# Kernel optimization log

Hardware: AMD Instinct MI355X
Metric: run time of the kernel (lower is better)

## Reference

```python
import jax, jax.numpy as jnp
import numpy as np

B, H, W, C, G = 4, 56, 56, 256, 16
K = 9  # 3x3 deformable kernel
GC = C // G


def _ln(x, g, b, eps=1e-5):
    mu = jnp.mean(x, axis=-1, keepdims=True)
    var = jnp.mean(jnp.square(x - mu), axis=-1, keepdims=True)
    return (x - mu) * jax.lax.rsqrt(var + eps) * g + b


def _gelu(x):
    return jax.nn.gelu(x, approximate=False)  # torch nn.GELU default = exact erf


def _dcnv3_core(x, offset, mask):
    # x: [B,H,W,C]; offset: [B,H,W,G*K*2] (x,y per point); mask: [B,H,W,G,K] softmaxed over K
    xg = x.reshape(B, H * W, G, GC)
    off = offset.reshape(B, H, W, G, K, 2)
    dy, dx = jnp.meshgrid(jnp.arange(-1.0, 2.0), jnp.arange(-1.0, 2.0), indexing="ij")
    dx = dx.reshape(K).astype(x.dtype)
    dy = dy.reshape(K).astype(x.dtype)
    gx = jnp.arange(W, dtype=x.dtype)[None, None, :, None, None]
    gy = jnp.arange(H, dtype=x.dtype)[None, :, None, None, None]
    # sampling locations in unpadded pixel coords (zeros outside image == F.pad + zero grid_sample)
    px = gx + dx + off[..., 0]  # [B,H,W,G,K]
    py = gy + dy + off[..., 1]

    def flat(p):  # [B,H,W,G,K] -> [B, H*W*K, G]
        return p.transpose(0, 1, 2, 4, 3).reshape(B, H * W * K, G)

    pxf, pyf = flat(px), flat(py)
    x0 = jnp.floor(pxf)
    y0 = jnp.floor(pyf)
    acc = jnp.zeros((B, H * W * K, G, GC), x.dtype)
    for cx, cy in ((x0, y0), (x0 + 1, y0), (x0, y0 + 1), (x0 + 1, y0 + 1)):
        wgt = (1 - jnp.abs(pxf - cx)) * (1 - jnp.abs(pyf - cy))
        valid = ((cx >= 0) & (cx < W) & (cy >= 0) & (cy < H)).astype(x.dtype)
        idx = (jnp.clip(cy, 0, H - 1).astype(jnp.int32) * W
               + jnp.clip(cx, 0, W - 1).astype(jnp.int32))[..., None]  # [B,HWK,G,1]
        v = jnp.take_along_axis(xg, idx, axis=1)  # [B,HWK,G,GC]
        acc = acc + (wgt * valid)[..., None] * v
    mf = flat(mask)[..., None]  # [B,HWK,G,1]
    out = (acc * mf).reshape(B, H * W, K, G, GC).sum(axis=2)
    return out.reshape(B, H, W, C)


def _dcn(x, w_in, b_in, w_dw, b_dw, ln_dw_g, ln_dw_b, w_off, b_off,
         w_mask, b_mask, w_out, b_out):
    xp = x @ w_in + b_in  # input projection (value branch)
    x1 = jax.lax.conv_general_dilated(
        x, w_dw, window_strides=(1, 1), padding="SAME",
        dimension_numbers=("NHWC", "HWIO", "NHWC"), feature_group_count=C) + b_dw
    x1 = _gelu(_ln(x1, ln_dw_g, ln_dw_b))  # dw_conv -> LN -> GELU
    offset = x1 @ w_off + b_off  # [B,H,W,G*K*2]
    mask = jax.nn.softmax((x1 @ w_mask + b_mask).reshape(B, H, W, G, K), axis=-1)
    y = _dcnv3_core(xp, offset, mask)
    return y @ w_out + b_out


def _block(x, w_in, b_in, w_dw, b_dw, ln_dw_g, ln_dw_b, w_off, b_off,
           w_mask, b_mask, w_out, b_out, ln1_g, ln1_b,
           w_fc1, b_fc1, w_fc2, b_fc2, ln2_g, ln2_b, gamma1, gamma2):
    # post_norm=True: x = x + gamma1*LN1(dcn(x)); x = x + gamma2*LN2(mlp(x))
    y = _dcn(x, w_in, b_in, w_dw, b_dw, ln_dw_g, ln_dw_b, w_off, b_off,
             w_mask, b_mask, w_out, b_out)
    x = x + gamma1 * _ln(y, ln1_g, ln1_b)
    m = _gelu(x @ w_fc1 + b_fc1) @ w_fc2 + b_fc2  # MLP (dropout = identity)
    x = x + gamma2 * _ln(m, ln2_g, ln2_b)
    return x


def setup_inputs() -> dict:
    key = jax.random.key(0)
    ks = jax.random.split(key, 9)
    f = jnp.float32

    def rn(k, shape, s=0.02):
        return jax.random.normal(k, shape, dtype=f) * s

    return {
        "x": jax.random.normal(ks[0], (B, H, W, C), dtype=f),
        "w_in": rn(ks[1], (C, C)), "b_in": jnp.zeros((C,), f),
        "w_dw": rn(ks[2], (3, 3, 1, C), 0.1), "b_dw": jnp.zeros((C,), f),
        "ln_dw_g": jnp.ones((C,), f), "ln_dw_b": jnp.zeros((C,), f),
        "w_off": rn(ks[3], (C, G * K * 2)), "b_off": jnp.zeros((G * K * 2,), f),
        "w_mask": rn(ks[4], (C, G * K)), "b_mask": jnp.zeros((G * K,), f),
        "w_out": rn(ks[5], (C, C)), "b_out": jnp.zeros((C,), f),
        "ln1_g": jnp.ones((C,), f), "ln1_b": jnp.zeros((C,), f),
        "w_fc1": rn(ks[6], (C, C)), "b_fc1": jnp.zeros((C,), f),
        "w_fc2": rn(ks[7], (C, C)), "b_fc2": jnp.zeros((C,), f),
        "ln2_g": jnp.ones((C,), f), "ln2_b": jnp.zeros((C,), f),
        "gamma1": jnp.ones((C,), f), "gamma2": jnp.ones((C,), f),
    }


def reference(x, w_in, b_in, w_dw, b_dw, ln_dw_g, ln_dw_b, w_off, b_off,
              w_mask, b_mask, w_out, b_out, ln1_g, ln1_b,
              w_fc1, b_fc1, w_fc2, b_fc2, ln2_g, ln2_b, gamma1, gamma2):
    return _block(x, w_in, b_in, w_dw, b_dw, ln_dw_g, ln_dw_b, w_off, b_off,
                  w_mask, b_mask, w_out, b_out, ln1_g, ln1_b,
                  w_fc1, b_fc1, w_fc2, b_fc2, ln2_g, ln2_b, gamma1, gamma2)
```

## Files before the change

### kernel.cpp

```cpp
#include <hip/hip_runtime.h>
#include <math.h>

typedef unsigned short u16;
typedef unsigned int u32;
typedef __attribute__((ext_vector_type(8))) short short8;
typedef __attribute__((ext_vector_type(4))) float f32x4;

#define NB 4
#define NH 56
#define NW 56
#define HW2 (NH*NW)
#define NPIX (NB*HW2)

__device__ __forceinline__ u16 f2b(float f) {
  union { float f; u32 u; } a; a.f = f;
  return (u16)((a.u + 0x7FFFu + ((a.u >> 16) & 1u)) >> 16);
}
__device__ __forceinline__ float b2f(u16 v) {
  union { u32 u; float f; } a; a.u = ((u32)v) << 16; return a.f;
}
__device__ __forceinline__ float gelu_exact(float v) {
  return 0.5f * v * (1.0f + erff(v * 0.70710678118654752f));
}
__device__ __forceinline__ int xcd_swz(int bid, int nwg) {
  const int q = nwg >> 3, r = nwg & 7, x = bid & 7, j = bid >> 3;
  return (x < r ? x * (q + 1) : r * (q + 1) + (x - r) * q) + j;
}
__device__ __forceinline__ u32 swz(int r, int b) {
  return (u32)(r * 512 + ((b ^ (r & 7)) << 4));
}

__global__ __launch_bounds__(256) void k1_kernel(
    const float* __restrict__ w_in, const float* __restrict__ w_out,
    const float* __restrict__ w_fc1, const float* __restrict__ w_fc2,
    const float* __restrict__ w_off, const float* __restrict__ w_mask,
    const float* __restrict__ b_off, const float* __restrict__ b_mask,
    u16* __restrict__ wT, float* __restrict__ bias_cat,
    const float* __restrict__ xf, const float* __restrict__ wdw,
    const float* __restrict__ bdw, const float* __restrict__ lng,
    const float* __restrict__ lnb, u16* __restrict__ x1)
{
  const int blk = blockIdx.x, t = threadIdx.x;
  if (blk < 1456) {
    const float* src; int n, N;
    if      (blk < 256)  { src = w_in;   n = blk;        N = 256; }
    else if (blk < 512)  { src = w_out;  n = blk - 256;  N = 256; }
    else if (blk < 768)  { src = w_fc1;  n = blk - 512;  N = 256; }
    else if (blk < 1024) { src = w_fc2;  n = blk - 768;  N = 256; }
    else if (blk < 1312) { src = w_off;  n = blk - 1024; N = 288; }
    else                 { src = w_mask; n = blk - 1312; N = 144; }
    wT[blk * 256 + t] = f2b(src[t * N + n]);
  } else if (blk == 1456) {
    for (int j = t; j < 432; j += 256)
      bias_cat[j] = (j < 288) ? b_off[j] : b_mask[j - 288];
  } else {
    const int pb = xcd_swz(blk - 1457, 3136);
    const int p = pb * 4 + (t >> 6);
    const int lane = t & 63, c0 = lane * 4;
    const int bb = p / HW2, hw = p - bb * HW2;
    const int h = hw / NW, w = hw - h * NW;
    float4 bd = *(const float4*)(bdw + c0);
    float a0 = bd.x, a1 = bd.y, a2 = bd.z, a3 = bd.w;
    #pragma unroll
    for (int kh = 0; kh < 3; ++kh) {
      const int hh = h + kh - 1;
      if ((unsigned)hh >= NH) continue;
      #pragma unroll
      for (int kw = 0; kw < 3; ++kw) {
        const int ww = w + kw - 1;
        if ((unsigned)ww >= NW) continue;
        float4 v = *(const float4*)(xf + (size_t)(bb * HW2 + hh * NW + ww) * 256 + c0);
        float4 wv = *(const float4*)(wdw + (kh * 3 + kw) * 256 + c0);
        a0 += v.x * wv.x; a1 += v.y * wv.y;
        a2 += v.z * wv.z; a3 += v.w * wv.w;
      }
    }
    float s1 = a0 + a1 + a2 + a3;
    float s2 = a0 * a0 + a1 * a1 + a2 * a2 + a3 * a3;
    #pragma unroll
    for (int d = 1; d < 64; d <<= 1) { s1 += __shfl_xor(s1, d); s2 += __shfl_xor(s2, d); }
    const float mu = s1 * (1.0f / 256.0f);
    const float var = s2 * (1.0f / 256.0f) - mu * mu;
    const float rs = rsqrtf(var + 1e-5f);
    float4 lg4 = *(const float4*)(lng + c0);
    float4 lb4 = *(const float4*)(lnb + c0);
    ushort4 o;
    o.x = f2b(gelu_exact((a0 - mu) * rs * lg4.x + lb4.x));
    o.y = f2b(gelu_exact((a1 - mu) * rs * lg4.y + lb4.y));
    o.z = f2b(gelu_exact((a2 - mu) * rs * lg4.z + lb4.z));
    o.w = f2b(gelu_exact((a3 - mu) * rs * lg4.w + lb4.w));
    *(ushort4*)(x1 + (size_t)p * 256 + c0) = o;
  }
}

template<int AF32>
__device__ __forceinline__ void gemm64_body(
    const void* __restrict__ Asrc, const u16* __restrict__ Brows,
    const float* __restrict__ bias, u16* __restrict__ Cout,
    int Ntot, int m0, int n0, char* As, char* Bs, int t)
{
  if (AF32) {
    const int r = t >> 2;
    const float4* src = (const float4*)((const float*)Asrc + (size_t)(m0 + r) * 256);
    #pragma unroll
    for (int i = 0; i < 16; ++i) {
      const int f4 = (t & 3) + i * 4;
      float4 v = src[f4];
      uint2 pk;
      pk.x = (u32)f2b(v.x) | ((u32)f2b(v.y) << 16);
      pk.y = (u32)f2b(v.z) | ((u32)f2b(v.w) << 16);
      *(uint2*)(As + swz(r, f4 >> 1) + (f4 & 1) * 8) = pk;
    }
  } else {
    const int r = t >> 2, c0 = t & 3;
    const u16* Ag = (const u16*)Asrc + (size_t)(m0 + r) * 256;
    #pragma unroll
    for (int i = 0; i < 8; ++i) {
      const int b = c0 + i * 4;
      *(uint4*)(As + swz(r, b)) = *(const uint4*)(Ag + b * 8);
    }
  }
  {
    const int r = t >> 2, c0 = t & 3;
    const int nrow = n0 + r;
    const u16* Bg = Brows + (size_t)nrow * 256;
    const bool bok = nrow < Ntot;
    #pragma unroll
    for (int i = 0; i < 8; ++i) {
      const int b = c0 + i * 4;
      uint4 bv = make_uint4(0u, 0u, 0u, 0u);
      if (bok) bv = *(const uint4*)(Bg + b * 8);
      *(uint4*)(Bs + swz(r, b)) = bv;
    }
  }
  __syncthreads();
  const int l = t & 63, w = t >> 6;
  const int wm = (w >> 1) << 5, wn = (w & 1) << 5;
  const int lr = l & 15, lk = l >> 4;
  const int ra0 = wm + lr, ra1 = wm + 16 + lr;
  const int rb0 = wn + lr, rb1 = wn + 16 + lr;
  f32x4 acc00 = {}, acc01 = {}, acc10 = {}, acc11 = {};
  #pragma unroll
  for (int ks = 0; ks < 8; ++ks) {
    const int bb = ks * 4 + lk;
    short8 a0 = *(const short8*)(As + swz(ra0, bb));
    short8 a1 = *(const short8*)(As + swz(ra1, bb));
    short8 b0 = *(const short8*)(Bs + swz(rb0, bb));
    short8 b1 = *(const short8*)(Bs + swz(rb1, bb));
    acc00 = __builtin_amdgcn_mfma_f32_16x16x32_bf16(a0, b0, acc00, 0, 0, 0);
    acc01 = __builtin_amdgcn_mfma_f32_16x16x32_bf16(a0, b1, acc01, 0, 0, 0);
    acc10 = __builtin_amdgcn_mfma_f32_16x16x32_bf16(a1, b0, acc10, 0, 0, 0);
    acc11 = __builtin_amdgcn_mfma_f32_16x16x32_bf16(a1, b1, acc11, 0, 0, 0);
  }
  const f32x4 accs[2][2] = {{acc00, acc01}, {acc10, acc11}};
  #pragma unroll
  for (int mi = 0; mi < 2; ++mi)
    #pragma unroll
    for (int ni = 0; ni < 2; ++ni) {
      const int col = n0 + wn + ni * 16 + lr;
      if (col < Ntot) {
        const float bv = bias[col];
        #pragma unroll
        for (int r4 = 0; r4 < 4; ++r4) {
          const int row = m0 + wm + mi * 16 + lk * 4 + r4;
          Cout[(size_t)row * Ntot + col] = f2b(accs[mi][ni][r4] + bv);
        }
      }
    }
}

__global__ __launch_bounds__(256) void k2_kernel(
    const float* __restrict__ xf, const u16* __restrict__ x1,
    const u16* __restrict__ wT, const float* __restrict__ b_in,
    const float* __restrict__ bcat, u16* __restrict__ xp_bf,
    u16* __restrict__ omb)
{
  __shared__ u16 lds[32768];
  char* As = (char*)lds;
  char* Bs = (char*)(lds + 16384);
  const int t = threadIdx.x;
  if (blockIdx.x < 784) {
    const int sb = xcd_swz(blockIdx.x, 784);
    const int m0 = (sb >> 2) * 64, n0 = (sb & 3) * 64;
    gemm64_body<1>(xf, wT, b_in, xp_bf, 256, m0, n0, As, Bs, t);
  } else {
    const int sb = xcd_swz((int)blockIdx.x - 784, 1372);
    const int m0 = (sb / 7) * 64, n0 = (sb % 7) * 64;
    gemm64_body<0>(x1, wT + 1024 * 256, bcat, omb, 432, m0, n0, As, Bs, t);
  }
}

__global__ __launch_bounds__(512) void dcn_tail_kernel(
    const u16* __restrict__ xp, const u16* __restrict__ omb,
    const u16* __restrict__ wT, const float* __restrict__ x,
    const float* __restrict__ b_out, const float* __restrict__ gamma1,
    const float* __restrict__ ln1g, const float* __restrict__ ln1b,
    const float* __restrict__ b_fc1, const float* __restrict__ b_fc2,
    const float* __restrict__ gamma2, const float* __restrict__ ln2g,
    const float* __restrict__ ln2b, float* __restrict__ out)
{
  __shared__ u16 As[32 * 256];
  __shared__ u16 lom[32 * 432];
  __shared__ float redS[32][8], redQ[32][8];
  const int t = threadIdx.x;
  const int blk = xcd_swz(blockIdx.x, 392);
  const int p0 = blk * 32;

  for (int i = t; i < 1728; i += 512) {
    const int row = i / 54, u = i - row * 54;
    *(uint4*)(lom + row * 432 + u * 8) =
        *(const uint4*)(omb + (size_t)(p0 + row) * 432 + u * 8);
  }
  __syncthreads();

  {
    const int lp = t >> 4, g = t & 15;
    const int p = p0 + lp;
    const int bb = p / HW2, hw = p - bb * HW2;
    const int h = hw / NW, w = hw - h * NW;
    const u16* off = lom + lp * 432 + g * 18;
    const u16* mk  = lom + lp * 432 + 288 + g * 9;
    float lg[9];
    float mx = -1e30f;
    #pragma unroll
    for (int k = 0; k < 9; ++k) { lg[k] = b2f(mk[k]); mx = fmaxf(mx, lg[k]); }
    float se = 0.0f;
    #pragma unroll
    for (int k = 0; k < 9; ++k) { lg[k] = __expf(lg[k] - mx); se += lg[k]; }
    const float inv = 1.0f / se;
    float a[16];
    #pragma unroll
    for (int j = 0; j < 16; ++j) a[j] = 0.f;
    const u16* gbase = xp + (size_t)bb * HW2 * 256 + g * 16;
    auto corner = [&](int cx, int cy, float wt) {
      if (cx < 0 || cx >= NW || cy < 0 || cy >= NH) return;
      const u16* vp = gbase + (size_t)(cy * NW + cx) * 256;
      uint4 v0 = *(const uint4*)vp;
      uint4 v1 = *(const uint4*)(vp + 8);
      const u32 wv[8] = {v0.x, v0.y, v0.z, v0.w, v1.x, v1.y, v1.z, v1.w};
      #pragma unroll
      for (int j = 0; j < 8; ++j) {
        union { u32 u; float f; } lo, hi;
        lo.u = wv[j] << 16; hi.u = wv[j] & 0xffff0000u;
        a[2 * j]     += wt * lo.f;
        a[2 * j + 1] += wt * hi.f;
      }
    };
    #pragma unroll
    for (int k = 0; k < 9; ++k) {
      const float px = (float)(w + (k % 3) - 1) + b2f(off[2 * k]);
      const float py = (float)(h + (k / 3) - 1) + b2f(off[2 * k + 1]);
      const float fx = floorf(px), fy = floorf(py);
      const int ix = (int)fx, iy = (int)fy;
      const float ax = px - fx, ay = py - fy;
      const float mwt = lg[k] * inv;
      corner(ix,     iy,     (1.0f - ax) * (1.0f - ay) * mwt);
      corner(ix + 1, iy,     ax * (1.0f - ay) * mwt);
      corner(ix,     iy + 1, (1.0f - ax) * ay * mwt);
      corner(ix + 1, iy + 1, ax * ay * mwt);
    }
    u16 tmp[16];
    #pragma unroll
    for (int j = 0; j < 16; ++j) tmp[j] = f2b(a[j]);
    const int u0 = g * 2;
    *(uint4*)((char*)As + lp * 512 + (((u0    ) ^ (lp & 7)) << 4)) = *(const uint4*)(tmp);
    *(uint4*)((char*)As + lp * 512 + (((u0 + 1) ^ (lp & 7)) << 4)) = *(const uint4*)(tmp + 8);
  }
  __syncthreads();

  const int l = t & 63, w8 = t >> 6;
  const int lr = l & 15, lk = l >> 4;
  const int colb = w8 * 32 + lr;
  f32x4 acc[2][2];
  auto do_gemm = [&](const u16* Bt) {
    #pragma unroll
    for (int mi = 0; mi < 2; ++mi)
      #pragma unroll
      for (int ni = 0; ni < 2; ++ni) acc[mi][ni] = (f32x4){0.f, 0.f, 0.f, 0.f};
    const u16* Bbase = Bt + (size_t)(w8 * 32 + lr) * 256 + lk * 8;
    #pragma unroll
    for (int ks = 0; ks < 8; ++ks) {
      short8 a0 = *(const short8*)((char*)As + swz(lr,      ks * 4 + lk));
      short8 a1 = *(const short8*)((char*)As + swz(16 + lr, ks * 4 + lk));
      #pragma unroll
      for (int ni = 0; ni < 2; ++ni) {
        short8 b = *(const short8*)(Bbase + ni * 16 * 256 + ks * 32);
        acc[0][ni] = __builtin_amdgcn_mfma_f32_16x16x32_bf16(a0, b, acc[0][ni], 0, 0, 0);
        acc[1][ni] = __builtin_amdgcn_mfma_f32_16x16x32_bf16(a1, b, acc[1][ni], 0, 0, 0);
      }
    }
  };
  auto lds_write_b16 = [&](int row, int col, u16 v) {
    *(u16*)((char*)As + row * 512 + (((col >> 3) ^ (row & 7)) << 4) + (col & 7) * 2) = v;
  };
  auto ln_reduce = [&](const float bv[2]) {
    float s1[2][4], s2[2][4];
    #pragma unroll
    for (int mi = 0; mi < 2; ++mi)
      #pragma unroll
      for (int r4 = 0; r4 < 4; ++r4) {
        float s = 0.f, q = 0.f;
        #pragma unroll
        for (int ni = 0; ni < 2; ++ni) {
          const float v = acc[mi][ni][r4] + bv[ni];
          s += v; q += v * v;
        }
        s1[mi][r4] = s; s2[mi][r4] = q;
      }
    #pragma unroll
    for (int d = 1; d < 16; d <<= 1)
      #pragma unroll
      for (int mi = 0; mi < 2; ++mi)
        #pragma unroll
        for (int r4 = 0; r4 < 4; ++r4) {
          s1[mi][r4] += __shfl_xor(s1[mi][r4], d);
          s2[mi][r4] += __shfl_xor(s2[mi][r4], d);
        }
    if (lr == 0) {
      #pragma unroll
      for (int mi = 0; mi < 2; ++mi)
        #pragma unroll
        for (int r4 = 0; r4 < 4; ++r4) {
          const int rl = mi * 16 + lk * 4 + r4;
          redS[rl][w8] = s1[mi][r4];
          redQ[rl][w8] = s2[mi][r4];
        }
    }
    __syncthreads();
  };
  auto row_stats = [&](int rl, float& mu, float& rs) {
    float S = 0.f, Q = 0.f;
    #pragma unroll
    for (int j = 0; j < 8; ++j) { S += redS[rl][j]; Q += redQ[rl][j]; }
    mu = S * (1.0f / 256.0f);
    const float var = Q * (1.0f / 256.0f) - mu * mu;
    rs = rsqrtf(var + 1e-5f);
  };

  do_gemm(wT + 256 * 256);
  float bv1[2] = {b_out[colb], b_out[colb + 16]};
  ln_reduce(bv1);

  float x2r[2][4][2];
  {
    const float gm[2]  = {gamma1[colb], gamma1[colb + 16]};
    const float lgv[2] = {ln1g[colb],   ln1g[colb + 16]};
    const float lbv[2] = {ln1b[colb],   ln1b[colb + 16]};
    #pragma unroll
    for (int mi = 0; mi < 2; ++mi)
      #pragma unroll
      for (int r4 = 0; r4 < 4; ++r4) {
        const int rl = mi * 16 + lk * 4 + r4;
        float mu, rs; row_stats(rl, mu, rs);
        const int row = p0 + rl;
        #pragma unroll
        for (int ni = 0; ni < 2; ++ni) {
          const float v = acc[mi][ni][r4] + bv1[ni];
          const float o = x[(size_t)row * 256 + colb + ni * 16]
                        + gm[ni] * ((v - mu) * rs * lgv[ni] + lbv[ni]);
          x2r[mi][r4][ni] = o;
          lds_write_b16(rl, colb + ni * 16, f2b(o));
        }
      }
  }
  __syncthreads();

  do_gemm(wT + 512 * 256);
  float m1v[2][4][2];
  const float bf1[2] = {b_fc1[colb], b_fc1[colb + 16]};
  #pragma unroll
  for (int mi = 0; mi < 2; ++mi)
    #pragma unroll
    for (int r4 = 0; r4 < 4; ++r4)
      #pragma unroll
      for (int ni = 0; ni < 2; ++ni)
        m1v[mi][r4][ni] = gelu_exact(acc[mi][ni][r4] + bf1[ni]);
  __syncthreads();
  #pragma unroll
  for (int mi = 0; mi < 2; ++mi)
    #pragma unroll
    for (int r4 = 0; r4 < 4; ++r4) {
      const int rl = mi * 16 + lk * 4 + r4;
      #pragma unroll
      for (int ni = 0; ni < 2; ++ni)
        lds_write_b16(rl, colb + ni * 16, f2b(m1v[mi][r4][ni]));
    }
  __syncthreads();

  do_gemm(wT + 768 * 256);
  float bv3[2] = {b_fc2[colb], b_fc2[colb + 16]};
  ln_reduce(bv3);
  {
    const float gm[2]  = {gamma2[colb], gamma2[colb + 16]};
    const float lgv[2] = {ln2g[colb],   ln2g[colb + 16]};
    const float lbv[2] = {ln2b[colb],   ln2b[colb + 16]};
    #pragma unroll
    for (int mi = 0; mi < 2; ++mi)
      #pragma unroll
      for (int r4 = 0; r4 < 4; ++r4) {
        const int rl = mi * 16 + lk * 4 + r4;
        float mu, rs; row_stats(rl, mu, rs);
        const int row = p0 + rl;
        #pragma unroll
        for (int ni = 0; ni < 2; ++ni) {
          const float v = acc[mi][ni][r4] + bv3[ni];
          out[(size_t)row * 256 + colb + ni * 16] =
              x2r[mi][r4][ni] + gm[ni] * ((v - mu) * rs * lgv[ni] + lbv[ni]);
        }
      }
  }
}

static constexpr size_t OFF_WT  = 0;
static constexpr size_t OFF_BC  = 745472;
static constexpr size_t OFF_XP  = 747520;
static constexpr size_t OFF_X1  = 7170048;
static constexpr size_t OFF_OMB = 13592576;

extern "C" void kernel_launch(void* const* d_in, const int* in_sizes, int n_in,
                              void* d_out, int out_size, void* d_ws, size_t ws_size,
                              hipStream_t stream)
{
  const float* x      = (const float*)d_in[0];
  const float* w_in   = (const float*)d_in[1];
  const float* b_in   = (const float*)d_in[2];
  const float* w_dw   = (const float*)d_in[3];
  const float* b_dw   = (const float*)d_in[4];
  const float* ln_dw_g= (const float*)d_in[5];
  const float* ln_dw_b= (const float*)d_in[6];
  const float* w_off  = (const float*)d_in[7];
  const float* b_off  = (const float*)d_in[8];
  const float* w_mask = (const float*)d_in[9];
  const float* b_mask = (const float*)d_in[10];
  const float* w_out  = (const float*)d_in[11];
  const float* b_out  = (const float*)d_in[12];
  const float* ln1_g  = (const float*)d_in[13];
  const float* ln1_b  = (const float*)d_in[14];
  const float* w_fc1  = (const float*)d_in[15];
  const float* b_fc1  = (const float*)d_in[16];
  const float* w_fc2  = (const float*)d_in[17];
  const float* b_fc2  = (const float*)d_in[18];
  const float* ln2_g  = (const float*)d_in[19];
  const float* ln2_b  = (const float*)d_in[20];
  const float* gamma1 = (const float*)d_in[21];
  const float* gamma2 = (const float*)d_in[22];
  float* out = (float*)d_out;

  char* ws = (char*)d_ws;
  u16*   wT    = (u16*)  (ws + OFF_WT);
  float* bcat  = (float*)(ws + OFF_BC);
  u16*   xp_bf = (u16*)  (ws + OFF_XP);
  u16*   x1    = (u16*)  (ws + OFF_X1);
  u16*   omb   = (u16*)  (ws + OFF_OMB);

  k1_kernel<<<dim3(1457 + 3136), 256, 0, stream>>>(
      w_in, w_out, w_fc1, w_fc2, w_off, w_mask, b_off, b_mask, wT, bcat,
      x, w_dw, b_dw, ln_dw_g, ln_dw_b, x1);
  k2_kernel<<<dim3(784 + 1372), 256, 0, stream>>>(
      x, x1, wT, b_in, bcat, xp_bf, omb);
  dcn_tail_kernel<<<dim3(392), 512, 0, stream>>>(
      xp_bf, omb, wT, x, b_out, gamma1, ln1_g, ln1_b, b_fc1, b_fc2,
      gamma2, ln2_g, ln2_b, out);
}
```

Before: 88.09 us.

## Halve tail-kernel tile to 16 pixels per block with 256 threads

The fused DCN tail kernel now handles 16 pixels per block with 4 waves instead of 32 pixels with 8 waves, launching 784 blocks instead of 392. Each wave now computes a 16x64 output slice with four MFMA accumulators in place of a 32x32 slice. The aim is to fill all compute units on the 256-CU device, since 392 blocks left many idle. In exchange, each block re-reads the weight matrices from global or L2 for fewer rows, roughly doubling weight traffic per pixel.

```diff
diff --git a/kernel.cpp b/kernel.cpp
--- a/kernel.cpp
+++ b/kernel.cpp
@@ -190,7 +190,7 @@
   }
 }
 
-__global__ __launch_bounds__(512) void dcn_tail_kernel(
+__global__ __launch_bounds__(256) void dcn_tail_kernel(
     const u16* __restrict__ xp, const u16* __restrict__ omb,
     const u16* __restrict__ wT, const float* __restrict__ x,
     const float* __restrict__ b_out, const float* __restrict__ gamma1,
@@ -199,14 +199,14 @@
     const float* __restrict__ gamma2, const float* __restrict__ ln2g,
     const float* __restrict__ ln2b, float* __restrict__ out)
 {
-  __shared__ u16 As[32 * 256];
-  __shared__ u16 lom[32 * 432];
-  __shared__ float redS[32][8], redQ[32][8];
+  __shared__ u16 As[16 * 256];
+  __shared__ u16 lom[16 * 432];
+  __shared__ float redS[16][4], redQ[16][4];
   const int t = threadIdx.x;
-  const int blk = xcd_swz(blockIdx.x, 392);
-  const int p0 = blk * 32;
-
-  for (int i = t; i < 1728; i += 512) {
+  const int blk = xcd_swz(blockIdx.x, 784);
+  const int p0 = blk * 16;
+
+  for (int i = t; i < 864; i += 256) {
     const int row = i / 54, u = i - row * 54;
     *(uint4*)(lom + row * 432 + u * 8) =
         *(const uint4*)(omb + (size_t)(p0 + row) * 432 + u * 8);
@@ -268,146 +268,143 @@
   }
   __syncthreads();
 
-  const int l = t & 63, w8 = t >> 6;
+  const int l = t & 63, w4 = t >> 6;
   const int lr = l & 15, lk = l >> 4;
-  const int colb = w8 * 32 + lr;
-  f32x4 acc[2][2];
+  const int colb = w4 * 64 + lr;
+  f32x4 acc[4];
   auto do_gemm = [&](const u16* Bt) {
     #pragma unroll
-    for (int mi = 0; mi < 2; ++mi)
-      #pragma unroll
-      for (int ni = 0; ni < 2; ++ni) acc[mi][ni] = (f32x4){0.f, 0.f, 0.f, 0.f};
-    const u16* Bbase = Bt + (size_t)(w8 * 32 + lr) * 256 + lk * 8;
+    for (int ni = 0; ni < 4; ++ni) acc[ni] = (f32x4){0.f, 0.f, 0.f, 0.f};
+    const u16* Bbase = Bt + (size_t)(w4 * 64 + lr) * 256 + lk * 8;
     #pragma unroll
     for (int ks = 0; ks < 8; ++ks) {
-      short8 a0 = *(const short8*)((char*)As + swz(lr,      ks * 4 + lk));
-      short8 a1 = *(const short8*)((char*)As + swz(16 + lr, ks * 4 + lk));
-      #pragma unroll
-      for (int ni = 0; ni < 2; ++ni) {
+      short8 a0 = *(const short8*)((char*)As + swz(lr, ks * 4 + lk));
+      #pragma unroll
+      for (int ni = 0; ni < 4; ++ni) {
         short8 b = *(const short8*)(Bbase + ni * 16 * 256 + ks * 32);
-        acc[0][ni] = __builtin_amdgcn_mfma_f32_16x16x32_bf16(a0, b, acc[0][ni], 0, 0, 0);
-        acc[1][ni] = __builtin_amdgcn_mfma_f32_16x16x32_bf16(a1, b, acc[1][ni], 0, 0, 0);
+        acc[ni] = __builtin_amdgcn_mfma_f32_16x16x32_bf16(a0, b, acc[ni], 0, 0, 0);
       }
     }
   };
   auto lds_write_b16 = [&](int row, int col, u16 v) {
     *(u16*)((char*)As + row * 512 + (((col >> 3) ^ (row & 7)) << 4) + (col & 7) * 2) = v;
   };
-  auto ln_reduce = [&](const float bv[2]) {
-    float s1[2][4], s2[2][4];
-    #pragma unroll
-    for (int mi = 0; mi < 2; ++mi)
+  auto ln_reduce = [&](const float bv[4]) {
+    float s1[4], s2[4];
+    #pragma unroll
+    for (int r4 = 0; r4 < 4; ++r4) {
+      float s = 0.f, q = 0.f;
+      #pragma unroll
+      for (int ni = 0; ni < 4; ++ni) {
+        const float v = acc[ni][r4] + bv[ni];
+        s += v; q += v * v;
+      }
+      s1[r4] = s; s2[r4] = q;
+    }
+    #pragma unroll
+    for (int d = 1; d < 16; d <<= 1)
       #pragma unroll
       for (int r4 = 0; r4 < 4; ++r4) {
-        float s = 0.f, q = 0.f;
-        #pragma unroll
-        for (int ni = 0; ni < 2; ++ni) {
-          const float v = acc[mi][ni][r4] + bv[ni];
-          s += v; q += v * v;
-        }
-        s1[mi][r4] = s; s2[mi][r4] = q;
-      }
-    #pragma unroll
-    for (int d = 1; d < 16; d <<= 1)
-      #pragma unroll
-      for (int mi = 0; mi < 2; ++mi)
-        #pragma unroll
-        for (int r4 = 0; r4 < 4; ++r4) {
-          s1[mi][r4] += __shfl_xor(s1[mi][r4], d);
-          s2[mi][r4] += __shfl_xor(s2[mi][r4], d);
-        }
+        s1[r4] += __shfl_xor(s1[r4], d);
+        s2[r4] += __shfl_xor(s2[r4], d);
+      }
     if (lr == 0) {
       #pragma unroll
-      for (int mi = 0; mi < 2; ++mi)
-        #pragma unroll
-        for (int r4 = 0; r4 < 4; ++r4) {
-          const int rl = mi * 16 + lk * 4 + r4;
-          redS[rl][w8] = s1[mi][r4];
-          redQ[rl][w8] = s2[mi][r4];
-        }
+      for (int r4 = 0; r4 < 4; ++r4) {
+        const int rl = lk * 4 + r4;
+        redS[rl][w4] = s1[r4];
+        redQ[rl][w4] = s2[r4];
+      }
     }
     __syncthreads();
   };
   auto row_stats = [&](int rl, float& mu, float& rs) {
-    float S = 0.f, Q = 0.f;
-    #pragma unroll
-    for (int j = 0; j < 8; ++j) { S += redS[rl][j]; Q += redQ[rl][j]; }
+    const float S = redS[rl][0] + redS[rl][1] + redS[rl][2] + redS[rl][3];
+    const float Q = redQ[rl][0] + redQ[rl][1] + redQ[rl][2] + redQ[rl][3];
     mu = S * (1.0f / 256.0f);
     const float var = Q * (1.0f / 256.0f) - mu * mu;
     rs = rsqrtf(var + 1e-5f);
   };
 
   do_gemm(wT + 256 * 256);
-  float bv1[2] = {b_out[colb], b_out[colb + 16]};
+  float bv1[4];
+  #pragma unroll
+  for (int ni = 0; ni < 4; ++ni) bv1[ni] = b_out[colb + ni * 16];
   ln_reduce(bv1);
 
-  float x2r[2][4][2];
+  float x2r[4][4];
   {
-    const float gm[2]  = {gamma1[colb], gamma1[colb + 16]};
-    const float lgv[2] = {ln1g[colb],   ln1g[colb + 16]};
-    const float lbv[2] = {ln1b[colb],   ln1b[colb + 16]};
-    #pragma unroll
-    for (int mi = 0; mi < 2; ++mi)
-      #pragma unroll
-      for (int r4 = 0; r4 < 4; ++r4) {
-        const int rl = mi * 16 + lk * 4 + r4;
-        float mu, rs; row_stats(rl, mu, rs);
-        const int row = p0 + rl;
-        #pragma unroll
-        for (int ni = 0; ni < 2; ++ni) {
-          const float v = acc[mi][ni][r4] + bv1[ni];
-          const float o = x[(size_t)row * 256 + colb + ni * 16]
-                        + gm[ni] * ((v - mu) * rs * lgv[ni] + lbv[ni]);
-          x2r[mi][r4][ni] = o;
-          lds_write_b16(rl, colb + ni * 16, f2b(o));
-        }
-      }
+    float gm[4], lgv[4], lbv[4];
+    #pragma unroll
+    for (int ni = 0; ni < 4; ++ni) {
+      gm[ni]  = gamma1[colb + ni * 16];
+      lgv[ni] = ln1g[colb + ni * 16];
+      lbv[ni] = ln1b[colb + ni * 16];
+    }
+    #pragma unroll
+    for (int r4 = 0; r4 < 4; ++r4) {
+      const int rl = lk * 4 + r4;
+      float mu, rs; row_stats(rl, mu, rs);
+      const int row = p0 + rl;
+      #pragma unroll
+      for (int ni = 0; ni < 4; ++ni) {
+        const float v = acc[ni][r4] + bv1[ni];
+        const float o = x[(size_t)row * 256 + colb + ni * 16]
+                      + gm[ni] * ((v - mu) * rs * lgv[ni] + lbv[ni]);
+        x2r[r4][ni] = o;
+        lds_write_b16(rl, colb + ni * 16, f2b(o));
+      }
+    }
   }
   __syncthreads();
 
   do_gemm(wT + 512 * 256);
-  float m1v[2][4][2];
-  const float bf1[2] = {b_fc1[colb], b_fc1[colb + 16]};
+  float m1v[4][4];
+  {
+    float bf1[4];
+    #pragma unroll
+    for (int ni = 0; ni < 4; ++ni) bf1[ni] = b_fc1[colb + ni * 16];
+    #pragma unroll
+    for (int r4 = 0; r4 < 4; ++r4)
+      #pragma unroll
+      for (int ni = 0; ni < 4; ++ni)
+        m1v[r4][ni] = gelu_exact(acc[ni][r4] + bf1[ni]);
+  }
+  __syncthreads();
   #pragma unroll
-  for (int mi = 0; mi < 2; ++mi)
-    #pragma unroll
-    for (int r4 = 0; r4 < 4; ++r4)
-      #pragma unroll
-      for (int ni = 0; ni < 2; ++ni)
-        m1v[mi][r4][ni] = gelu_exact(acc[mi][ni][r4] + bf1[ni]);
-  __syncthreads();
+  for (int r4 = 0; r4 < 4; ++r4) {
+    const int rl = lk * 4 + r4;
+    #pragma unroll
+    for (int ni = 0; ni < 4; ++ni)
+      lds_write_b16(rl, colb + ni * 16, f2b(m1v[r4][ni]));
+  }
+  __syncthreads();
+
+  do_gemm(wT + 768 * 256);
+  float bv3[4];
   #pragma unroll
-  for (int mi = 0; mi < 2; ++mi)
-    #pragma unroll
-    for (int r4 = 0; r4 < 4; ++r4) {
-      const int rl = mi * 16 + lk * 4 + r4;
-      #pragma unroll
-      for (int ni = 0; ni < 2; ++ni)
-        lds_write_b16(rl, colb + ni * 16, f2b(m1v[mi][r4][ni]));
-    }
-  __syncthreads();
-
-  do_gemm(wT + 768 * 256);
-  float bv3[2] = {b_fc2[colb], b_fc2[colb + 16]};
+  for (int ni = 0; ni < 4; ++ni) bv3[ni] = b_fc2[colb + ni * 16];
   ln_reduce(bv3);
   {
-    const float gm[2]  = {gamma2[colb], gamma2[colb + 16]};
-    const float lgv[2] = {ln2g[colb],   ln2g[colb + 16]};
-    const float lbv[2] = {ln2b[colb],   ln2b[colb + 16]};
-    #pragma unroll
-    for (int mi = 0; mi < 2; ++mi)
-      #pragma unroll
-      for (int r4 = 0; r4 < 4; ++r4) {
-        const int rl = mi * 16 + lk * 4 + r4;
-        float mu, rs; row_stats(rl, mu, rs);
-        const int row = p0 + rl;
-        #pragma unroll
-        for (int ni = 0; ni < 2; ++ni) {
-          const float v = acc[mi][ni][r4] + bv3[ni];
-          out[(size_t)row * 256 + colb + ni * 16] =
-              x2r[mi][r4][ni] + gm[ni] * ((v - mu) * rs * lgv[ni] + lbv[ni]);
-        }
-      }
+    float gm[4], lgv[4], lbv[4];
+    #pragma unroll
+    for (int ni = 0; ni < 4; ++ni) {
+      gm[ni]  = gamma2[colb + ni * 16];
+      lgv[ni] = ln2g[colb + ni * 16];
+      lbv[ni] = ln2b[colb + ni * 16];
+    }
+    #pragma unroll
+    for (int r4 = 0; r4 < 4; ++r4) {
+      const int rl = lk * 4 + r4;
+      float mu, rs; row_stats(rl, mu, rs);
+      const int row = p0 + rl;
+      #pragma unroll
+      for (int ni = 0; ni < 4; ++ni) {
+        const float v = acc[ni][r4] + bv3[ni];
+        out[(size_t)row * 256 + colb + ni * 16] =
+            x2r[r4][ni] + gm[ni] * ((v - mu) * rs * lgv[ni] + lbv[ni]);
+      }
+    }
   }
 }
 
@@ -458,7 +455,7 @@
       x, w_dw, b_dw, ln_dw_g, ln_dw_b, x1);
   k2_kernel<<<dim3(784 + 1372), 256, 0, stream>>>(
       x, x1, wT, b_in, bcat, xp_bf, omb);
-  dcn_tail_kernel<<<dim3(392), 512, 0, stream>>>(
+  dcn_tail_kernel<<<dim3(784), 256, 0, stream>>>(
       xp_bf, omb, wT, x, b_out, gamma1, ln1_g, ln1_b, b_fc1, b_fc2,
       gamma2, ln2_g, ln2_b, out);
 }
```

Result: slower. 109.3 us (+24.0%).

## Double tail kernel threads to 1024, splitting gather and GEMM columns finer

Applied to the files above, without the earlier changes.

The DCN tail kernel now runs 1024 threads per block instead of 512. Each bilinear-gather thread handles half of a group's 16 channels (one 16-byte load per corner), and each wave in the fused GEMM/LN chain owns 16 output columns instead of 32. The reduction scratch grows to 16 partials per row. This raises memory-level parallelism for the gather with only 392 blocks, at the cost of more LN reduction work, more redundant offset/softmax math per thread, and larger blocks that may limit occupancy.

```diff
diff --git a/kernel.cpp b/kernel.cpp
--- a/kernel.cpp
+++ b/kernel.cpp
@@ -190,7 +190,7 @@
   }
 }
 
-__global__ __launch_bounds__(512) void dcn_tail_kernel(
+__global__ __launch_bounds__(1024) void dcn_tail_kernel(
     const u16* __restrict__ xp, const u16* __restrict__ omb,
     const u16* __restrict__ wT, const float* __restrict__ x,
     const float* __restrict__ b_out, const float* __restrict__ gamma1,
@@ -201,12 +201,12 @@
 {
   __shared__ u16 As[32 * 256];
   __shared__ u16 lom[32 * 432];
-  __shared__ float redS[32][8], redQ[32][8];
+  __shared__ float redS[32][16], redQ[32][16];
   const int t = threadIdx.x;
   const int blk = xcd_swz(blockIdx.x, 392);
   const int p0 = blk * 32;
 
-  for (int i = t; i < 1728; i += 512) {
+  for (int i = t; i < 1728; i += 1024) {
     const int row = i / 54, u = i - row * 54;
     *(uint4*)(lom + row * 432 + u * 8) =
         *(const uint4*)(omb + (size_t)(p0 + row) * 432 + u * 8);
@@ -214,7 +214,8 @@
   __syncthreads();
 
   {
-    const int lp = t >> 4, g = t & 15;
+    const int lp = t >> 5, gh = t & 31;
+    const int g = gh >> 1, hf = gh & 1;
     const int p = p0 + lp;
     const int bb = p / HW2, hw = p - bb * HW2;
     const int h = hw / NW, w = hw - h * NW;
@@ -228,18 +229,14 @@
     #pragma unroll
     for (int k = 0; k < 9; ++k) { lg[k] = __expf(lg[k] - mx); se += lg[k]; }
     const float inv = 1.0f / se;
-    float a[16];
-    #pragma unroll
-    for (int j = 0; j < 16; ++j) a[j] = 0.f;
-    const u16* gbase = xp + (size_t)bb * HW2 * 256 + g * 16;
+    float a[8] = {0.f,0.f,0.f,0.f,0.f,0.f,0.f,0.f};
+    const u16* gbase = xp + (size_t)bb * HW2 * 256 + g * 16 + hf * 8;
     auto corner = [&](int cx, int cy, float wt) {
       if (cx < 0 || cx >= NW || cy < 0 || cy >= NH) return;
-      const u16* vp = gbase + (size_t)(cy * NW + cx) * 256;
-      uint4 v0 = *(const uint4*)vp;
-      uint4 v1 = *(const uint4*)(vp + 8);
-      const u32 wv[8] = {v0.x, v0.y, v0.z, v0.w, v1.x, v1.y, v1.z, v1.w};
-      #pragma unroll
-      for (int j = 0; j < 8; ++j) {
+      uint4 v = *(const uint4*)(gbase + (size_t)(cy * NW + cx) * 256);
+      const u32 wv[4] = {v.x, v.y, v.z, v.w};
+      #pragma unroll
+      for (int j = 0; j < 4; ++j) {
         union { u32 u; float f; } lo, hi;
         lo.u = wv[j] << 16; hi.u = wv[j] & 0xffff0000u;
         a[2 * j]     += wt * lo.f;
@@ -259,53 +256,41 @@
       corner(ix,     iy + 1, (1.0f - ax) * ay * mwt);
       corner(ix + 1, iy + 1, ax * ay * mwt);
     }
-    u16 tmp[16];
-    #pragma unroll
-    for (int j = 0; j < 16; ++j) tmp[j] = f2b(a[j]);
-    const int u0 = g * 2;
-    *(uint4*)((char*)As + lp * 512 + (((u0    ) ^ (lp & 7)) << 4)) = *(const uint4*)(tmp);
-    *(uint4*)((char*)As + lp * 512 + (((u0 + 1) ^ (lp & 7)) << 4)) = *(const uint4*)(tmp + 8);
-  }
-  __syncthreads();
-
-  const int l = t & 63, w8 = t >> 6;
+    u16 tmp[8];
+    #pragma unroll
+    for (int j = 0; j < 8; ++j) tmp[j] = f2b(a[j]);
+    *(uint4*)((char*)As + lp * 512 + ((gh ^ (lp & 7)) << 4)) = *(const uint4*)(tmp);
+  }
+  __syncthreads();
+
+  const int l = t & 63, wv16 = t >> 6;
   const int lr = l & 15, lk = l >> 4;
-  const int colb = w8 * 32 + lr;
-  f32x4 acc[2][2];
+  const int colb = wv16 * 16 + lr;
+  f32x4 acc[2];
   auto do_gemm = [&](const u16* Bt) {
-    #pragma unroll
-    for (int mi = 0; mi < 2; ++mi)
-      #pragma unroll
-      for (int ni = 0; ni < 2; ++ni) acc[mi][ni] = (f32x4){0.f, 0.f, 0.f, 0.f};
-    const u16* Bbase = Bt + (size_t)(w8 * 32 + lr) * 256 + lk * 8;
+    acc[0] = (f32x4){0.f, 0.f, 0.f, 0.f};
+    acc[1] = (f32x4){0.f, 0.f, 0.f, 0.f};
+    const u16* Bbase = Bt + (size_t)colb * 256 + lk * 8;
     #pragma unroll
     for (int ks = 0; ks < 8; ++ks) {
       short8 a0 = *(const short8*)((char*)As + swz(lr,      ks * 4 + lk));
       short8 a1 = *(const short8*)((char*)As + swz(16 + lr, ks * 4 + lk));
-      #pragma unroll
-      for (int ni = 0; ni < 2; ++ni) {
-        short8 b = *(const short8*)(Bbase + ni * 16 * 256 + ks * 32);
-        acc[0][ni] = __builtin_amdgcn_mfma_f32_16x16x32_bf16(a0, b, acc[0][ni], 0, 0, 0);
-        acc[1][ni] = __builtin_amdgcn_mfma_f32_16x16x32_bf16(a1, b, acc[1][ni], 0, 0, 0);
-      }
+      short8 b = *(const short8*)(Bbase + ks * 32);
+      acc[0] = __builtin_amdgcn_mfma_f32_16x16x32_bf16(a0, b, acc[0], 0, 0, 0);
+      acc[1] = __builtin_amdgcn_mfma_f32_16x16x32_bf16(a1, b, acc[1], 0, 0, 0);
     }
   };
   auto lds_write_b16 = [&](int row, int col, u16 v) {
     *(u16*)((char*)As + row * 512 + (((col >> 3) ^ (row & 7)) << 4) + (col & 7) * 2) = v;
   };
-  auto ln_reduce = [&](const float bv[2]) {
+  auto ln_reduce = [&](float bv) {
     float s1[2][4], s2[2][4];
     #pragma unroll
     for (int mi = 0; mi < 2; ++mi)
       #pragma unroll
       for (int r4 = 0; r4 < 4; ++r4) {
-        float s = 0.f, q = 0.f;
-        #pragma unroll
-        for (int ni = 0; ni < 2; ++ni) {
-          const float v = acc[mi][ni][r4] + bv[ni];
-          s += v; q += v * v;
-        }
-        s1[mi][r4] = s; s2[mi][r4] = q;
+        const float v = acc[mi][r4] + bv;
+        s1[mi][r4] = v; s2[mi][r4] = v * v;
       }
     #pragma unroll
     for (int d = 1; d < 16; d <<= 1)
@@ -322,8 +307,8 @@
         #pragma unroll
         for (int r4 = 0; r4 < 4; ++r4) {
           const int rl = mi * 16 + lk * 4 + r4;
-          redS[rl][w8] = s1[mi][r4];
-          redQ[rl][w8] = s2[mi][r4];
+          redS[rl][wv16] = s1[mi][r4];
+          redQ[rl][wv16] = s2[mi][r4];
         }
     }
     __syncthreads();
@@ -331,21 +316,21 @@
   auto row_stats = [&](int rl, float& mu, float& rs) {
     float S = 0.f, Q = 0.f;
     #pragma unroll
-    for (int j = 0; j < 8; ++j) { S += redS[rl][j]; Q += redQ[rl][j]; }
+    for (int j = 0; j < 16; ++j) { S += redS[rl][j]; Q += redQ[rl][j]; }
     mu = S * (1.0f / 256.0f);
     const float var = Q * (1.0f / 256.0f) - mu * mu;
     rs = rsqrtf(var + 1e-5f);
   };
 
   do_gemm(wT + 256 * 256);
-  float bv1[2] = {b_out[colb], b_out[colb + 16]};
+  const float bv1 = b_out[colb];
   ln_reduce(bv1);
 
-  float x2r[2][4][2];
+  float x2r[2][4];
   {
-    const float gm[2]  = {gamma1[colb], gamma1[colb + 16]};
-    const float lgv[2] = {ln1g[colb],   ln1g[colb + 16]};
-    const float lbv[2] = {ln1b[colb],   ln1b[colb + 16]};
+    const float gm  = gamma1[colb];
+    const float lgv = ln1g[colb];
+    const float lbv = ln1b[colb];
     #pragma unroll
     for (int mi = 0; mi < 2; ++mi)
       #pragma unroll
@@ -353,47 +338,42 @@
         const int rl = mi * 16 + lk * 4 + r4;
         float mu, rs; row_stats(rl, mu, rs);
         const int row = p0 + rl;
-        #pragma unroll
-        for (int ni = 0; ni < 2; ++ni) {
-          const float v = acc[mi][ni][r4] + bv1[ni];
-          const float o = x[(size_t)row * 256 + colb + ni * 16]
-                        + gm[ni] * ((v - mu) * rs * lgv[ni] + lbv[ni]);
-          x2r[mi][r4][ni] = o;
-          lds_write_b16(rl, colb + ni * 16, f2b(o));
-        }
+        const float v = acc[mi][r4] + bv1;
+        const float o = x[(size_t)row * 256 + colb]
+                      + gm * ((v - mu) * rs * lgv + lbv);
+        x2r[mi][r4] = o;
+        lds_write_b16(rl, colb, f2b(o));
       }
   }
   __syncthreads();
 
   do_gemm(wT + 512 * 256);
-  float m1v[2][4][2];
-  const float bf1[2] = {b_fc1[colb], b_fc1[colb + 16]};
+  float m1v[2][4];
+  {
+    const float bf1 = b_fc1[colb];
+    #pragma unroll
+    for (int mi = 0; mi < 2; ++mi)
+      #pragma unroll
+      for (int r4 = 0; r4 < 4; ++r4)
+        m1v[mi][r4] = gelu_exact(acc[mi][r4] + bf1);
+  }
+  __syncthreads();
   #pragma unroll
   for (int mi = 0; mi < 2; ++mi)
     #pragma unroll
-    for (int r4 = 0; r4 < 4; ++r4)
-      #pragma unroll
-      for (int ni = 0; ni < 2; ++ni)
-        m1v[mi][r4][ni] = gelu_exact(acc[mi][ni][r4] + bf1[ni]);
-  __syncthreads();
-  #pragma unroll
-  for (int mi = 0; mi < 2; ++mi)
-    #pragma unroll
     for (int r4 = 0; r4 < 4; ++r4) {
       const int rl = mi * 16 + lk * 4 + r4;
-      #pragma unroll
-      for (int ni = 0; ni < 2; ++ni)
-        lds_write_b16(rl, colb + ni * 16, f2b(m1v[mi][r4][ni]));
+      lds_write_b16(rl, colb, f2b(m1v[mi][r4]));
     }
   __syncthreads();
 
   do_gemm(wT + 768 * 256);
-  float bv3[2] = {b_fc2[colb], b_fc2[colb + 16]};
+  const float bv3 = b_fc2[colb];
   ln_reduce(bv3);
   {
-    const float gm[2]  = {gamma2[colb], gamma2[colb + 16]};
-    const float lgv[2] = {ln2g[colb],   ln2g[colb + 16]};
-    const float lbv[2] = {ln2b[colb],   ln2b[colb + 16]};
+    const float gm  = gamma2[colb];
+    const float lgv = ln2g[colb];
+    const float lbv = ln2b[colb];
     #pragma unroll
     for (int mi = 0; mi < 2; ++mi)
       #pragma unroll
@@ -401,12 +381,9 @@
         const int rl = mi * 16 + lk * 4 + r4;
         float mu, rs; row_stats(rl, mu, rs);
         const int row = p0 + rl;
-        #pragma unroll
-        for (int ni = 0; ni < 2; ++ni) {
-          const float v = acc[mi][ni][r4] + bv3[ni];
-          out[(size_t)row * 256 + colb + ni * 16] =
-              x2r[mi][r4][ni] + gm[ni] * ((v - mu) * rs * lgv[ni] + lbv[ni]);
-        }
+        const float v = acc[mi][r4] + bv3;
+        out[(size_t)row * 256 + colb] =
+            x2r[mi][r4] + gm * ((v - mu) * rs * lgv + lbv);
       }
   }
 }
@@ -458,7 +435,7 @@
       x, w_dw, b_dw, ln_dw_g, ln_dw_b, x1);
   k2_kernel<<<dim3(784 + 1372), 256, 0, stream>>>(
       x, x1, wT, b_in, bcat, xp_bf, omb);
-  dcn_tail_kernel<<<dim3(392), 512, 0, stream>>>(
+  dcn_tail_kernel<<<dim3(392), 1024, 0, stream>>>(
       xp_bf, omb, wT, x, b_out, gamma1, ln1_g, ln1_b, b_fc1, b_fc2,
       gamma2, ln2_g, ln2_b, out);
 }
```

After: 120.4 us. 1.37x slower.

## Restructure k2 GEMMs to full-width N per block with B read from global

Applied to the files above, without the earlier changes.

The k2 GEMM kernel now gives each 512-thread block a 64-row tile covering the full output width (256 for the input projection, 432 for offset/mask), replacing the many 64x64 tiles. Only the A rows are staged in LDS and converted once per row block, so A is loaded and bf16-converted once instead of 4 or 7 times. B fragments are read straight from global memory (L2/L1-resident weights) instead of being staged through LDS. This cuts redundant A traffic and launch count, but leaves only 392 blocks, lowers occupancy, and relies on cache hits for the global weight loads.

```diff
diff --git a/kernel.cpp b/kernel.cpp
--- a/kernel.cpp
+++ b/kernel.cpp
@@ -93,100 +93,97 @@
   }
 }
 
-template<int AF32>
-__device__ __forceinline__ void gemm64_body(
-    const void* __restrict__ Asrc, const u16* __restrict__ Brows,
-    const float* __restrict__ bias, u16* __restrict__ Cout,
-    int Ntot, int m0, int n0, char* As, char* Bs, int t)
-{
-  if (AF32) {
-    const int r = t >> 2;
-    const float4* src = (const float4*)((const float*)Asrc + (size_t)(m0 + r) * 256);
-    #pragma unroll
-    for (int i = 0; i < 16; ++i) {
-      const int f4 = (t & 3) + i * 4;
-      float4 v = src[f4];
-      uint2 pk;
-      pk.x = (u32)f2b(v.x) | ((u32)f2b(v.y) << 16);
-      pk.y = (u32)f2b(v.z) | ((u32)f2b(v.w) << 16);
-      *(uint2*)(As + swz(r, f4 >> 1) + (f4 & 1) * 8) = pk;
-    }
-  } else {
-    const int r = t >> 2, c0 = t & 3;
-    const u16* Ag = (const u16*)Asrc + (size_t)(m0 + r) * 256;
-    #pragma unroll
-    for (int i = 0; i < 8; ++i) {
-      const int b = c0 + i * 4;
-      *(uint4*)(As + swz(r, b)) = *(const uint4*)(Ag + b * 8);
-    }
-  }
-  {
-    const int r = t >> 2, c0 = t & 3;
-    const int nrow = n0 + r;
-    const u16* Bg = Brows + (size_t)nrow * 256;
-    const bool bok = nrow < Ntot;
-    #pragma unroll
-    for (int i = 0; i < 8; ++i) {
-      const int b = c0 + i * 4;
-      uint4 bv = make_uint4(0u, 0u, 0u, 0u);
-      if (bok) bv = *(const uint4*)(Bg + b * 8);
-      *(uint4*)(Bs + swz(r, b)) = bv;
-    }
-  }
-  __syncthreads();
-  const int l = t & 63, w = t >> 6;
-  const int wm = (w >> 1) << 5, wn = (w & 1) << 5;
-  const int lr = l & 15, lk = l >> 4;
-  const int ra0 = wm + lr, ra1 = wm + 16 + lr;
-  const int rb0 = wn + lr, rb1 = wn + 16 + lr;
-  f32x4 acc00 = {}, acc01 = {}, acc10 = {}, acc11 = {};
-  #pragma unroll
-  for (int ks = 0; ks < 8; ++ks) {
-    const int bb = ks * 4 + lk;
-    short8 a0 = *(const short8*)(As + swz(ra0, bb));
-    short8 a1 = *(const short8*)(As + swz(ra1, bb));
-    short8 b0 = *(const short8*)(Bs + swz(rb0, bb));
-    short8 b1 = *(const short8*)(Bs + swz(rb1, bb));
-    acc00 = __builtin_amdgcn_mfma_f32_16x16x32_bf16(a0, b0, acc00, 0, 0, 0);
-    acc01 = __builtin_amdgcn_mfma_f32_16x16x32_bf16(a0, b1, acc01, 0, 0, 0);
-    acc10 = __builtin_amdgcn_mfma_f32_16x16x32_bf16(a1, b0, acc10, 0, 0, 0);
-    acc11 = __builtin_amdgcn_mfma_f32_16x16x32_bf16(a1, b1, acc11, 0, 0, 0);
-  }
-  const f32x4 accs[2][2] = {{acc00, acc01}, {acc10, acc11}};
-  #pragma unroll
-  for (int mi = 0; mi < 2; ++mi)
-    #pragma unroll
-    for (int ni = 0; ni < 2; ++ni) {
-      const int col = n0 + wn + ni * 16 + lr;
-      if (col < Ntot) {
-        const float bv = bias[col];
-        #pragma unroll
-        for (int r4 = 0; r4 < 4; ++r4) {
-          const int row = m0 + wm + mi * 16 + lk * 4 + r4;
-          Cout[(size_t)row * Ntot + col] = f2b(accs[mi][ni][r4] + bv);
-        }
-      }
-    }
-}
-
-__global__ __launch_bounds__(256) void k2_kernel(
+__global__ __launch_bounds__(512) void k2_kernel(
     const float* __restrict__ xf, const u16* __restrict__ x1,
     const u16* __restrict__ wT, const float* __restrict__ b_in,
     const float* __restrict__ bcat, u16* __restrict__ xp_bf,
     u16* __restrict__ omb)
 {
-  __shared__ u16 lds[32768];
-  char* As = (char*)lds;
-  char* Bs = (char*)(lds + 16384);
+  __shared__ u16 As[64 * 256];
   const int t = threadIdx.x;
-  if (blockIdx.x < 784) {
-    const int sb = xcd_swz(blockIdx.x, 784);
-    const int m0 = (sb >> 2) * 64, n0 = (sb & 3) * 64;
-    gemm64_body<1>(xf, wT, b_in, xp_bf, 256, m0, n0, As, Bs, t);
+  const int l = t & 63, w = t >> 6;
+  const int lr = l & 15, lk = l >> 4;
+  const int wm = w >> 2, wn = w & 3;
+  const int ra0 = wm * 32 + lr, ra1 = wm * 32 + 16 + lr;
+  if (blockIdx.x < 196) {
+    const int m0 = xcd_swz(blockIdx.x, 196) * 64;
+    {
+      const int r = t >> 3;
+      const float4* src = (const float4*)(xf + (size_t)(m0 + r) * 256);
+      #pragma unroll
+      for (int i = 0; i < 8; ++i) {
+        const int f4 = (t & 7) + i * 8;
+        float4 v = src[f4];
+        uint2 pk;
+        pk.x = (u32)f2b(v.x) | ((u32)f2b(v.y) << 16);
+        pk.y = (u32)f2b(v.z) | ((u32)f2b(v.w) << 16);
+        *(uint2*)((char*)As + swz(r, f4 >> 1) + (f4 & 1) * 8) = pk;
+      }
+    }
+    __syncthreads();
+    f32x4 acc[2][4] = {};
+    const u16* Bbase = wT + (size_t)(wn * 64 + lr) * 256 + lk * 8;
+    #pragma unroll
+    for (int ks = 0; ks < 8; ++ks) {
+      short8 a0 = *(const short8*)((char*)As + swz(ra0, ks * 4 + lk));
+      short8 a1 = *(const short8*)((char*)As + swz(ra1, ks * 4 + lk));
+      #pragma unroll
+      for (int ni = 0; ni < 4; ++ni) {
+        short8 b = *(const short8*)(Bbase + ni * 16 * 256 + ks * 32);
+        acc[0][ni] = __builtin_amdgcn_mfma_f32_16x16x32_bf16(a0, b, acc[0][ni], 0, 0, 0);
+        acc[1][ni] = __builtin_amdgcn_mfma_f32_16x16x32_bf16(a1, b, acc[1][ni], 0, 0, 0);
+      }
+    }
+    const int colb = wn * 64 + lr;
+    #pragma unroll
+    for (int mi = 0; mi < 2; ++mi)
+      #pragma unroll
+      for (int r4 = 0; r4 < 4; ++r4) {
+        const int row = m0 + wm * 32 + mi * 16 + lk * 4 + r4;
+        #pragma unroll
+        for (int ni = 0; ni < 4; ++ni)
+          xp_bf[(size_t)row * 256 + colb + ni * 16] = f2b(acc[mi][ni][r4] + b_in[colb + ni * 16]);
+      }
   } else {
-    const int sb = xcd_swz((int)blockIdx.x - 784, 1372);
-    const int m0 = (sb / 7) * 64, n0 = (sb % 7) * 64;
-    gemm64_body<0>(x1, wT + 1024 * 256, bcat, omb, 432, m0, n0, As, Bs, t);
+    const int m0 = xcd_swz((int)blockIdx.x - 196, 196) * 64;
+    {
+      const int r = t >> 3, j0 = (t & 7) * 4;
+      const uint4* src = (const uint4*)(x1 + (size_t)(m0 + r) * 256);
+      #pragma unroll
+      for (int i = 0; i < 4; ++i)
+        *(uint4*)((char*)As + swz(r, j0 + i)) = src[j0 + i];
+    }
+    __syncthreads();
+    const int nt = (wn == 3) ? 6 : 7;
+    f32x4 acc[2][7] = {};
+    #pragma unroll
+    for (int ks = 0; ks < 8; ++ks) {
+      short8 a0 = *(const short8*)((char*)As + swz(ra0, ks * 4 + lk));
+      short8 a1 = *(const short8*)((char*)As + swz(ra1, ks * 4 + lk));
+      #pragma unroll
+      for (int ni = 0; ni < 7; ++ni) {
+        if (ni < nt) {
+          const int nrow = 1024 + (wn * 7 + ni) * 16 + lr;
+          short8 b = *(const short8*)(wT + (size_t)nrow * 256 + lk * 8 + ks * 32);
+          acc[0][ni] = __builtin_amdgcn_mfma_f32_16x16x32_bf16(a0, b, acc[0][ni], 0, 0, 0);
+          acc[1][ni] = __builtin_amdgcn_mfma_f32_16x16x32_bf16(a1, b, acc[1][ni], 0, 0, 0);
+        }
+      }
+    }
+    #pragma unroll
+    for (int ni = 0; ni < 7; ++ni) {
+      if (ni < nt) {
+        const int col = (wn * 7 + ni) * 16 + lr;
+        const float bv = bcat[col];
+        #pragma unroll
+        for (int mi = 0; mi < 2; ++mi)
+          #pragma unroll
+          for (int r4 = 0; r4 < 4; ++r4) {
+            const int row = m0 + wm * 32 + mi * 16 + lk * 4 + r4;
+            omb[(size_t)row * 432 + col] = f2b(acc[mi][ni][r4] + bv);
+          }
+      }
+    }
   }
 }
 
@@ -456,7 +453,7 @@
   k1_kernel<<<dim3(1457 + 3136), 256, 0, stream>>>(
       w_in, w_out, w_fc1, w_fc2, w_off, w_mask, b_off, b_mask, wT, bcat,
       x, w_dw, b_dw, ln_dw_g, ln_dw_b, x1);
-  k2_kernel<<<dim3(784 + 1372), 256, 0, stream>>>(
+  k2_kernel<<<dim3(196 + 196), 512, 0, stream>>>(
       x, x1, wT, b_in, bcat, xp_bf, omb);
   dcn_tail_kernel<<<dim3(392), 512, 0, stream>>>(
       xp_bf, omb, wT, x, b_out, gamma1, ln1_g, ln1_b, b_fc1, b_fc2,
```

New measurement: 94.75 us. +7.6%, slower.
